# Optimization experiments

Hardware: AMD Instinct MI355X
Metric: run time of the kernel (lower is better)

Reference implementation:

```python
import jax, jax.numpy as jnp
import numpy as np

B, N, D_IN, D_H, D_OUT = 32, 512, 512, 512, 512


def _xavier(key, fan_in, fan_out):
    bound = np.sqrt(6.0 / (fan_in + fan_out))
    return jax.random.uniform(key, (fan_in, fan_out), jnp.float32, -bound, bound)


def setup_inputs() -> dict:
    key = jax.random.key(0)
    ks = jax.random.split(key, 8)
    batch_graph = jax.random.normal(ks[0], (B, N, D_IN), jnp.float32)
    adj = jax.random.uniform(ks[1], (B, N, N), jnp.float32)  # per-graph adjacency blocks
    W0 = _xavier(ks[2], D_IN, D_H)
    b0 = jnp.zeros((D_H,), jnp.float32)
    W1 = _xavier(ks[3], D_H, D_H)
    b1 = jnp.zeros((D_H,), jnp.float32)
    W2 = _xavier(ks[4], D_H, D_OUT)
    b2 = jnp.zeros((D_OUT,), jnp.float32)
    return {"batch_graph": batch_graph, "adj": adj,
            "W0": W0, "b0": b0, "W1": W1, "b1": b1, "W2": W2, "b2": b2}


def _gcn_layer(h, adj, W, b):
    # GraphConvolution: adj @ (h @ W) + b, batched per graph.
    # Equivalent to big_adj @ (big_graph @ W) since big_adj is block-diagonal.
    support = jnp.einsum('bnd,de->bne', h, W)
    return jnp.einsum('bnm,bme->bne', adj, support) + b


def reference(batch_graph, adj, W0, b0, W1, b1, W2, b2):
    # dropout is identity at inference time
    h = jax.nn.relu(_gcn_layer(batch_graph, adj, W0, b0))
    h = jax.nn.relu(_gcn_layer(h, adj, W1, b1))
    h = _gcn_layer(h, adj, W2, b2)  # no activation on final layer
    return h  # [B, N, D_OUT] == torch.stack(big_graph.split(N))
```

## Files before the change

kernel.cpp:

```cpp
#include <hip/hip_runtime.h>
#include <stdint.h>

typedef __bf16 bf16x8 __attribute__((ext_vector_type(8)));
typedef float f32x4 __attribute__((ext_vector_type(4)));
typedef unsigned short u16x4 __attribute__((ext_vector_type(4)));

static __device__ __forceinline__ unsigned short f2bf(float f) {
    union { float f; unsigned u; } v; v.f = f;
    unsigned r = (v.u + 0x7FFFu + ((v.u >> 16) & 1u)) >> 16;
    return (unsigned short)r;
}

__global__ void prep_kernel(const float* __restrict__ X,
                            const float* __restrict__ adj,
                            const float* __restrict__ W0,
                            const float* __restrict__ W1,
                            const float* __restrict__ W2,
                            unsigned short* __restrict__ bufH,
                            unsigned short* __restrict__ adjB,
                            unsigned short* __restrict__ Wt) {
    const int bid = blockIdx.x;
    const int t = threadIdx.x;
    if (bid < 16384) {
        const float* src = (bid < 8192) ? X : adj;
        unsigned short* dst = (bid < 8192) ? bufH : adjB;
        const int i = (bid & 8191) * 256 + t;
        f32x4 v = ((const f32x4*)src)[i];
        u16x4 o;
        o.x = f2bf(v.x); o.y = f2bf(v.y); o.z = f2bf(v.z); o.w = f2bf(v.w);
        ((u16x4*)dst)[i] = o;
    } else {
        const int wb = bid - 16384;
        const int z = wb >> 8;
        const int tile = wb & 255;
        const float* W = (z == 0) ? W0 : (z == 1) ? W1 : W2;
        unsigned short* out = Wt + (size_t)z * (512 * 512);
        __shared__ float tileS[32][33];
        const int bx = (tile & 15) * 32, by = (tile >> 4) * 32;
        const int tx = t & 31, ty = t >> 5;
        #pragma unroll
        for (int r = 0; r < 32; r += 8)
            tileS[ty + r][tx] = W[(size_t)(by + ty + r) * 512 + (bx + tx)];
        __syncthreads();
        #pragma unroll
        for (int r = 0; r < 32; r += 8)
            out[(size_t)(bx + ty + r) * 512 + (by + tx)] = f2bf(tileS[tx][ty + r]);
    }
}

template<int LDA, int LDB, int LDO, bool BIAS, bool RELU, typename OT>
__global__ __launch_bounds__(256, 2)
void gemm_abT_ct(const unsigned short* __restrict__ A,
                 const unsigned short* __restrict__ B,
                 OT* __restrict__ out, const float* __restrict__ bias,
                 long batchA, long batchB, long batchO) {
    __shared__ unsigned short As[128 * 128];
    __shared__ unsigned short Bs[128 * 128];

    const int tid  = threadIdx.x;
    const int lane = tid & 63;
    const int wave = tid >> 6;
    const int quad = lane >> 4;
    const int l16  = lane & 15;
    const int wm   = wave & 1;
    const int wn   = wave >> 1;

    const int m0 = blockIdx.x * 128;
    const int n0 = blockIdx.y * 128;
    A   += (size_t)blockIdx.z * batchA;
    B   += (size_t)blockIdx.z * batchB;
    out += (size_t)blockIdx.z * batchO;

    const int trow = tid >> 4;
    const int tpos = (tid & 15) ^ trow;
    const unsigned short* aG = A + (size_t)(m0 + trow) * LDA + tpos * 8;
    const unsigned short* bG = B + (size_t)(n0 + trow) * LDB + tpos * 8;
    char* aL = (char*)As + tid * 16;
    char* bL = (char*)Bs + tid * 16;

    f32x4 acc[4][4];
    #pragma unroll
    for (int i = 0; i < 4; ++i)
        #pragma unroll
        for (int j = 0; j < 4; ++j) {
            f32x4 z = {0.f, 0.f, 0.f, 0.f};
            acc[i][j] = z;
        }

    #pragma unroll 1
    for (int kk = 0; kk < 4; ++kk) {
        const int ko = kk * 128;
        #pragma unroll
        for (int r = 0; r < 8; ++r) {
            __builtin_amdgcn_global_load_lds(
                (__attribute__((address_space(1))) void*)(uintptr_t)(aG + (size_t)(r * 16) * LDA + ko),
                (__attribute__((address_space(3))) void*)(aL + r * 4096), 16, 0, 0);
        }
        #pragma unroll
        for (int r = 0; r < 8; ++r) {
            __builtin_amdgcn_global_load_lds(
                (__attribute__((address_space(1))) void*)(uintptr_t)(bG + (size_t)(r * 16) * LDB + ko),
                (__attribute__((address_space(3))) void*)(bL + r * 4096), 16, 0, 0);
        }
        __syncthreads();

        #pragma unroll
        for (int ks = 0; ks < 4; ++ks) {
            bf16x8 af[4], bfr[4];
            #pragma unroll
            for (int i = 0; i < 4; ++i) {
                const int row = wm * 64 + i * 16 + l16;
                const int idx = row * 16 + ((ks * 4 + quad) ^ (row & 15));
                af[i] = *(const bf16x8*)((const char*)As + idx * 16);
            }
            #pragma unroll
            for (int j = 0; j < 4; ++j) {
                const int row = wn * 64 + j * 16 + l16;
                const int idx = row * 16 + ((ks * 4 + quad) ^ (row & 15));
                bfr[j] = *(const bf16x8*)((const char*)Bs + idx * 16);
            }
            #pragma unroll
            for (int i = 0; i < 4; ++i)
                #pragma unroll
                for (int j = 0; j < 4; ++j)
                    acc[i][j] = __builtin_amdgcn_mfma_f32_16x16x32_bf16(af[i], bfr[j], acc[i][j], 0, 0, 0);
        }
        __syncthreads();
    }

    #pragma unroll
    for (int i = 0; i < 4; ++i) {
        const int mb = m0 + wm * 64 + i * 16 + quad * 4;
        f32x4 bb = {0.f, 0.f, 0.f, 0.f};
        if constexpr (BIAS) bb = *(const f32x4*)(bias + mb);
        #pragma unroll
        for (int j = 0; j < 4; ++j) {
            const int n = n0 + wn * 64 + j * 16 + l16;
            f32x4 v = acc[i][j];
            if constexpr (BIAS) v += bb;
            if constexpr (RELU) {
                v.x = v.x > 0.f ? v.x : 0.f;
                v.y = v.y > 0.f ? v.y : 0.f;
                v.z = v.z > 0.f ? v.z : 0.f;
                v.w = v.w > 0.f ? v.w : 0.f;
            }
            if constexpr (sizeof(OT) == 4) {
                *(f32x4*)((float*)out + (size_t)n * LDO + mb) = v;
            } else {
                u16x4 o;
                o.x = f2bf(v.x); o.y = f2bf(v.y); o.z = f2bf(v.z); o.w = f2bf(v.w);
                *(u16x4*)((unsigned short*)out + (size_t)n * LDO + mb) = o;
            }
        }
    }
}

extern "C" void kernel_launch(void* const* d_in, const int* in_sizes, int n_in,
                              void* d_out, int out_size, void* d_ws, size_t ws_size,
                              hipStream_t stream) {
    (void)in_sizes; (void)n_in; (void)out_size; (void)ws_size;
    const float* X   = (const float*)d_in[0];
    const float* adj = (const float*)d_in[1];
    const float* W0  = (const float*)d_in[2];
    const float* b0  = (const float*)d_in[3];
    const float* W1  = (const float*)d_in[4];
    const float* b1  = (const float*)d_in[5];
    const float* W2  = (const float*)d_in[6];
    const float* b2  = (const float*)d_in[7];
    float* out = (float*)d_out;

    char* ws = (char*)d_ws;
    const size_t SZ = 16777216;
    unsigned short* adjB = (unsigned short*)(ws);
    unsigned short* bufH = (unsigned short*)(ws + SZ);
    unsigned short* tmpT = (unsigned short*)(ws + 2 * SZ);
    unsigned short* Wt   = (unsigned short*)(ws + 3 * SZ);
    const unsigned short* W0t = Wt;
    const unsigned short* W1t = Wt + 262144;
    const unsigned short* W2t = Wt + 2 * 262144;

    prep_kernel<<<16384 + 768, 256, 0, stream>>>(X, adj, W0, W1, W2, bufH, adjB, Wt);

    const long BATCH = 512L * 512L;

    gemm_abT_ct<512, 512, 16384, false, false, unsigned short>
        <<<dim3(128, 4, 1), 256, 0, stream>>>(bufH, W0t, tmpT, nullptr, 0, 0, 0);
    gemm_abT_ct<16384, 512, 512, true, true, unsigned short>
        <<<dim3(4, 4, 32), 256, 0, stream>>>(tmpT, adjB, bufH, b0, 512, BATCH, BATCH);
    gemm_abT_ct<512, 512, 16384, false, false, unsigned short>
        <<<dim3(128, 4, 1), 256, 0, stream>>>(bufH, W1t, tmpT, nullptr, 0, 0, 0);
    gemm_abT_ct<16384, 512, 512, true, true, unsigned short>
        <<<dim3(4, 4, 32), 256, 0, stream>>>(tmpT, adjB, bufH, b1, 512, BATCH, BATCH);
    gemm_abT_ct<512, 512, 16384, false, false, unsigned short>
        <<<dim3(128, 4, 1), 256, 0, stream>>>(bufH, W2t, tmpT, nullptr, 0, 0, 0);
    gemm_abT_ct<16384, 512, 512, true, false, float>
        <<<dim3(4, 4, 32), 256, 0, stream>>>(tmpT, adjB, out, b2, 512, BATCH, BATCH);
}
```

Before: 225.7 us.

## Double-buffer LDS tiles with K=64 stages to overlap loads and MFMA

Splits the 128x128 K-tile shared buffers into two 128x64 buffers and issues the async global-to-LDS loads for the next half-tile while computing on the current one. The swizzle pattern and load mapping are adapted to 8 chunks per row. The goal is to hide global memory latency behind MFMA work instead of stalling on a barrier every K-step. Total LDS stays the same, but there are twice as many barriers, and the syncthreads wait may still force load completion before compute.

```diff
diff --git a/kernel.cpp b/kernel.cpp
--- a/kernel.cpp
+++ b/kernel.cpp
@@ -54,8 +54,8 @@
                  const unsigned short* __restrict__ B,
                  OT* __restrict__ out, const float* __restrict__ bias,
                  long batchA, long batchB, long batchO) {
-    __shared__ unsigned short As[128 * 128];
-    __shared__ unsigned short Bs[128 * 128];
+    __shared__ unsigned short As[2][128 * 64];
+    __shared__ unsigned short Bs[2][128 * 64];
 
     const int tid  = threadIdx.x;
     const int lane = tid & 63;
@@ -71,12 +71,10 @@
     B   += (size_t)blockIdx.z * batchB;
     out += (size_t)blockIdx.z * batchO;
 
-    const int trow = tid >> 4;
-    const int tpos = (tid & 15) ^ trow;
-    const unsigned short* aG = A + (size_t)(m0 + trow) * LDA + tpos * 8;
-    const unsigned short* bG = B + (size_t)(n0 + trow) * LDB + tpos * 8;
-    char* aL = (char*)As + tid * 16;
-    char* bL = (char*)Bs + tid * 16;
+    const int trow8 = tid >> 3;
+    const int tpos8 = (tid & 7) ^ (trow8 & 7);
+    const unsigned short* aG = A + (size_t)(m0 + trow8) * LDA + tpos8 * 8;
+    const unsigned short* bG = B + (size_t)(n0 + trow8) * LDB + tpos8 * 8;
 
     f32x4 acc[4][4];
     #pragma unroll
@@ -87,46 +85,61 @@
             acc[i][j] = z;
         }
 
+#define STAGE(buf, ko)                                                         \
+    do {                                                                       \
+        char* aL = (char*)As[buf] + tid * 16;                                  \
+        char* bL = (char*)Bs[buf] + tid * 16;                                  \
+        _Pragma("unroll")                                                      \
+        for (int r = 0; r < 4; ++r)                                            \
+            __builtin_amdgcn_global_load_lds(                                  \
+                (__attribute__((address_space(1))) void*)(uintptr_t)(aG + (size_t)(r * 32) * LDA + (ko)), \
+                (__attribute__((address_space(3))) void*)(aL + r * 4096), 16, 0, 0); \
+        _Pragma("unroll")                                                      \
+        for (int r = 0; r < 4; ++r)                                            \
+            __builtin_amdgcn_global_load_lds(                                  \
+                (__attribute__((address_space(1))) void*)(uintptr_t)(bG + (size_t)(r * 32) * LDB + (ko)), \
+                (__attribute__((address_space(3))) void*)(bL + r * 4096), 16, 0, 0); \
+    } while (0)
+
+#define COMPUTE(buf)                                                           \
+    do {                                                                       \
+        _Pragma("unroll")                                                      \
+        for (int ks = 0; ks < 2; ++ks) {                                       \
+            bf16x8 af[4], bfr[4];                                              \
+            _Pragma("unroll")                                                  \
+            for (int i = 0; i < 4; ++i) {                                      \
+                const int row = wm * 64 + i * 16 + l16;                        \
+                const int idx = row * 8 + ((ks * 4 + quad) ^ (row & 7));       \
+                af[i] = *(const bf16x8*)((const char*)As[buf] + idx * 16);     \
+            }                                                                  \
+            _Pragma("unroll")                                                  \
+            for (int j = 0; j < 4; ++j) {                                      \
+                const int row = wn * 64 + j * 16 + l16;                        \
+                const int idx = row * 8 + ((ks * 4 + quad) ^ (row & 7));       \
+                bfr[j] = *(const bf16x8*)((const char*)Bs[buf] + idx * 16);    \
+            }                                                                  \
+            _Pragma("unroll")                                                  \
+            for (int i = 0; i < 4; ++i)                                        \
+                _Pragma("unroll")                                              \
+                for (int j = 0; j < 4; ++j)                                    \
+                    acc[i][j] = __builtin_amdgcn_mfma_f32_16x16x32_bf16(af[i], bfr[j], acc[i][j], 0, 0, 0); \
+        }                                                                      \
+    } while (0)
+
+    STAGE(0, 0);
+    __syncthreads();
+
     #pragma unroll 1
-    for (int kk = 0; kk < 4; ++kk) {
-        const int ko = kk * 128;
-        #pragma unroll
-        for (int r = 0; r < 8; ++r) {
-            __builtin_amdgcn_global_load_lds(
-                (__attribute__((address_space(1))) void*)(uintptr_t)(aG + (size_t)(r * 16) * LDA + ko),
-                (__attribute__((address_space(3))) void*)(aL + r * 4096), 16, 0, 0);
-        }
-        #pragma unroll
-        for (int r = 0; r < 8; ++r) {
-            __builtin_amdgcn_global_load_lds(
-                (__attribute__((address_space(1))) void*)(uintptr_t)(bG + (size_t)(r * 16) * LDB + ko),
-                (__attribute__((address_space(3))) void*)(bL + r * 4096), 16, 0, 0);
-        }
+    for (int kp = 0; kp < 4; ++kp) {
+        STAGE(1, kp * 128 + 64);
+        COMPUTE(0);
         __syncthreads();
-
-        #pragma unroll
-        for (int ks = 0; ks < 4; ++ks) {
-            bf16x8 af[4], bfr[4];
-            #pragma unroll
-            for (int i = 0; i < 4; ++i) {
-                const int row = wm * 64 + i * 16 + l16;
-                const int idx = row * 16 + ((ks * 4 + quad) ^ (row & 15));
-                af[i] = *(const bf16x8*)((const char*)As + idx * 16);
-            }
-            #pragma unroll
-            for (int j = 0; j < 4; ++j) {
-                const int row = wn * 64 + j * 16 + l16;
-                const int idx = row * 16 + ((ks * 4 + quad) ^ (row & 15));
-                bfr[j] = *(const bf16x8*)((const char*)Bs + idx * 16);
-            }
-            #pragma unroll
-            for (int i = 0; i < 4; ++i)
-                #pragma unroll
-                for (int j = 0; j < 4; ++j)
-                    acc[i][j] = __builtin_amdgcn_mfma_f32_16x16x32_bf16(af[i], bfr[j], acc[i][j], 0, 0, 0);
-        }
+        if (kp < 3) STAGE(0, kp * 128 + 128);
+        COMPUTE(1);
         __syncthreads();
     }
+#undef STAGE
+#undef COMPUTE
 
     #pragma unroll
     for (int i = 0; i < 4; ++i) {
```

Result: no change. 229.2 us (+1.5%).
